# Kernel optimization log

Hardware: AMD Instinct MI355X
Metric: run time of the kernel (lower is better)

## Reference

```python
import jax, jax.numpy as jnp
import numpy as np

B, IN_DIM, C, E, TOPK = 16384, 768, 50, 8, 2
RH = 256          # router hidden_dim
HS = [512, 256]   # expert hidden_sizes
THR = 0.05        # BitNet-1.58b ternarization threshold


def _xavier(k, shape):
    fan_out, fan_in = shape[-2], shape[-1]
    lim = float(np.sqrt(6.0 / (fan_in + fan_out)))
    return jax.random.uniform(k, shape, jnp.float32, -lim, lim)


def setup_inputs() -> dict:
    key = jax.random.key(0)
    ks = jax.random.split(key, 8)
    return {
        "x": jax.random.normal(ks[0], (B, IN_DIM), jnp.float32),
        # Router MLP: in_dim -> RH -> RH//2 -> E (torch Linear: W is (out,in))
        "rW1": _xavier(ks[1], (RH, IN_DIM)), "rb1": jnp.zeros((RH,), jnp.float32),
        "rW2": _xavier(ks[2], (RH // 2, RH)), "rb2": jnp.zeros((RH // 2,), jnp.float32),
        "rW3": _xavier(ks[3], (E, RH // 2)), "rb3": jnp.zeros((E,), jnp.float32),
        # Stacked expert weights: (E, out, in)
        "eW1": _xavier(ks[4], (E, HS[0], IN_DIM)), "eb1": jnp.zeros((E, HS[0]), jnp.float32),
        "eW2": _xavier(ks[5], (E, HS[1], HS[0])), "eb2": jnp.zeros((E, HS[1]), jnp.float32),
        "eW3": _xavier(ks[6], (E, C, HS[1])), "eb3": jnp.zeros((E, C), jnp.float32),
    }


def _ternary(W):
    # BitNet-1.58b: ternarize weights with |w|>threshold, scale by mean |W| per matrix
    scale = jnp.mean(jnp.abs(W), axis=(-2, -1), keepdims=True)
    Wq = jnp.sign(W) * (jnp.abs(W) > THR).astype(W.dtype)
    return Wq * scale


def reference(x, rW1, rb1, rW2, rb2, rW3, rb3, eW1, eb1, eW2, eb2, eW3, eb3):
    # ---- Router (eval mode: dropout = identity) ----
    h = jax.nn.relu(x @ rW1.T + rb1)
    h = jax.nn.relu(h @ rW2.T + rb2)
    router_logits = h @ rW3.T + rb3                      # (B, E)
    router_p = jax.nn.softmax(router_logits, axis=1)     # (B, E)

    # ---- Top-k gating; scatter gate weights back to dense (B, E) ----
    k_val, k_idx = jax.lax.top_k(router_p, TOPK)         # (B, K)
    rows = jnp.arange(x.shape[0])[:, None]
    gate = jnp.zeros_like(router_p).at[rows, k_idx].set(k_val)  # 0 for unselected experts

    # ---- Batched ternary-quantized expert MLPs (all experts, all samples) ----
    W1q, W2q, W3q = _ternary(eW1), _ternary(eW2), _ternary(eW3)
    a1 = jax.nn.relu(jnp.einsum('bd,ehd->ebh', x, W1q) + eb1[:, None, :])   # (E,B,H1)
    a2 = jax.nn.relu(jnp.einsum('ebh,egh->ebg', a1, W2q) + eb2[:, None, :]) # (E,B,H2)
    expert_logits = jnp.einsum('ebg,ecg->ebc', a2, W3q) + eb3[:, None, :]   # (E,B,C)

    # ---- Weighted combine over top-k experts (equivalent to the per-expert loop) ----
    out = jnp.einsum('ebc,be->bc', expert_logits, gate) / TOPK              # (B,C)

    lb_loss = jnp.float32(0.0)  # eval mode: self.training is False
    return (out, router_p, lb_loss)
```

## Files before the change

kernel.cpp:

```cpp
#include <hip/hip_runtime.h>
#include <hip/hip_bf16.h>

typedef __attribute__((ext_vector_type(4))) float f32x4;
typedef __attribute__((ext_vector_type(8))) short bf16x8;

#define B_ROWS 16384
#define IN_DIM 768
#define H1 512
#define H2 256
#define NC 50
#define NE 8
#define RH1 256
#define RH2 128
#define CHK 128

static __device__ __forceinline__ f32x4 mfma16(bf16x8 a, bf16x8 b, f32x4 c) {
    return __builtin_amdgcn_mfma_f32_16x16x32_bf16(a, b, c, 0, 0, 0);
}

typedef __attribute__((address_space(1))) const unsigned int gas_u32;
typedef __attribute__((address_space(3))) unsigned int las_u32;
static __device__ __forceinline__ void gl16(const void* g, void* l) {
    __builtin_amdgcn_global_load_lds((gas_u32*)g, (las_u32*)l, 16, 0, 0);
}

static __device__ __forceinline__ bf16x8 expand_frag(uint2 pw) {
    unsigned q0 = (pw.x & 0x01010101u) << 7;
    unsigned q1 = (pw.y & 0x01010101u) << 7;
    union { unsigned u[4]; bf16x8 v; } r;
    r.u[0] = __builtin_amdgcn_perm(pw.x, q0, 0x05010400u);
    r.u[1] = __builtin_amdgcn_perm(pw.x, q0, 0x07030602u);
    r.u[2] = __builtin_amdgcn_perm(pw.y, q1, 0x05010400u);
    r.u[3] = __builtin_amdgcn_perm(pw.y, q1, 0x07030602u);
    return r.v;
}

static __device__ __forceinline__ void decomp_f4(float4 v, ushort4* hv, ushort4* lv) {
    float vv[4] = {v.x, v.y, v.z, v.w};
    ushort ho[4], lo4[4];
    #pragma unroll
    for (int q = 0; q < 4; ++q) {
        __hip_bfloat16 h = __float2bfloat16(vv[q]);
        float hf = __bfloat162float(h);
        __hip_bfloat16 l = __float2bfloat16(vv[q] - hf);
        ho[q] = *(ushort*)&h; lo4[q] = *(ushort*)&l;
    }
    *hv = make_ushort4(ho[0], ho[1], ho[2], ho[3]);
    *lv = make_ushort4(lo4[0], lo4[1], lo4[2], lo4[3]);
}

static __device__ __forceinline__ ushort4 cvt_f4_bf16(float4 v) {
    float vv[4] = {v.x, v.y, v.z, v.w};
    ushort ho[4];
    #pragma unroll
    for (int q = 0; q < 4; ++q) {
        __hip_bfloat16 h = __float2bfloat16(vv[q]);
        ho[q] = *(ushort*)&h;
    }
    return make_ushort4(ho[0], ho[1], ho[2], ho[3]);
}

__global__ __launch_bounds__(512) void pack_absum_kernel(
    const float* __restrict__ eW1, const float* __restrict__ eW2, const float* __restrict__ eW3,
    unsigned char* __restrict__ W1p8, unsigned char* __restrict__ W2p8,
    unsigned char* __restrict__ W3p8,
    float* __restrict__ p1, float* __restrict__ p2, float* __restrict__ p3)
{
    const int mat = blockIdx.y >> 3, e = blockIdx.y & 7;
    const int u = blockIdx.x * 512 + threadIdx.x;
    const float* src; unsigned char* dst; int valid = 1; float* P; int np;
    if (mat == 0) {
        int lane = u & 63, nblk = (u >> 6) & 31, ks = u >> 11;
        int n = nblk * 16 + (lane & 15), k = ks * 32 + (lane >> 4) * 8;
        src = eW1 + ((size_t)e * H1 + n) * IN_DIM + k;
        dst = W1p8 + (size_t)e * 393216
            + (size_t)ks * 16384 + (nblk >> 1) * 1024 + lane * 16 + (nblk & 1) * 8;
        P = p1; np = 96;
    } else if (mat == 1) {
        if (u >= 16384) return;
        int lane = u & 63, nblk = (u >> 6) & 15, ks = u >> 10;
        int n = nblk * 16 + (lane & 15), k = ks * 32 + (lane >> 4) * 8;
        src = eW2 + ((size_t)e * H2 + n) * H1 + k;
        dst = W2p8 + (size_t)e * 131072
            + (size_t)ks * 8192 + (nblk >> 1) * 1024 + lane * 16 + (nblk & 1) * 8;
        P = p2; np = 32;
    } else {
        if (u >= 2048) return;
        int lane = u & 63, nblk = (u >> 6) & 3, ks = u >> 8;
        int n = nblk * 16 + (lane & 15), k = ks * 32 + (lane >> 4) * 8;
        valid = (n < NC);
        src = eW3 + ((size_t)e * NC + (valid ? n : 0)) * H2 + k;
        dst = W3p8 + ((size_t)e * 2048 + u) * 8;
        P = p3; np = 4;
    }
    unsigned lo = 0, hi = 0;
    float s = 0.f;
    #pragma unroll
    for (int j = 0; j < 4; ++j) {
        float w = valid ? src[j] : 0.f;
        s += fabsf(w);
        unsigned c = (fabsf(w) > 0.05f) ? (w > 0.f ? 0x3Fu : 0xBFu) : 0u;
        lo |= c << (8 * j);
    }
    #pragma unroll
    for (int j = 0; j < 4; ++j) {
        float w = valid ? src[4 + j] : 0.f;
        s += fabsf(w);
        unsigned c = (fabsf(w) > 0.05f) ? (w > 0.f ? 0x3Fu : 0xBFu) : 0u;
        hi |= c << (8 * j);
    }
    *(uint2*)dst = make_uint2(lo, hi);
    const int lane = threadIdx.x & 63, wave = threadIdx.x >> 6;
    #pragma unroll
    for (int o = 32; o; o >>= 1) s += __shfl_down(s, o);
    __shared__ float red[8];
    if (lane == 0) red[wave] = s;
    __syncthreads();
    if (threadIdx.x == 0) {
        float t = 0.f;
        #pragma unroll
        for (int i = 0; i < 8; ++i) t += red[i];
        P[e * np + blockIdx.x] = t;
    }
}

__global__ __launch_bounds__(64) void finalize_scales_kernel(
    const float* __restrict__ p1, const float* __restrict__ p2, const float* __restrict__ p3,
    float* __restrict__ s1, float* __restrict__ s2, float* __restrict__ s3,
    int* __restrict__ counts)
{
    int t = threadIdx.x;
    if (t < 8) {
        float a = 0.f;
        for (int i = 0; i < 96; ++i) a += p1[t * 96 + i];
        s1[t] = a / (float)(H1 * IN_DIM);
    } else if (t < 16) {
        int e = t - 8; float a = 0.f;
        for (int i = 0; i < 32; ++i) a += p2[e * 32 + i];
        s2[e] = a / (float)(H2 * H1);
    } else if (t < 24) {
        int e = t - 16; float a = 0.f;
        for (int i = 0; i < 4; ++i) a += p3[e * 4 + i];
        s3[e] = a / (float)(NC * H2);
    } else if (t < 32) {
        counts[t - 24] = 0;
    }
}

__global__ __launch_bounds__(512) void pack_router_kernel(
    const float* __restrict__ rW1, ushort* __restrict__ rw1hp, ushort* __restrict__ rw1lp,
    const float* __restrict__ rW2, ushort* __restrict__ rw2hp, ushort* __restrict__ rw2lp)
{
    int u = blockIdx.x * 512 + threadIdx.x;
    const float* src; ushort* dh; ushort* dl;
    if (u < 24576) {
        int lane = u & 63, nblk = (u >> 6) & 15, ks = u >> 10;
        int n = nblk * 16 + (lane & 15), k = ks * 32 + (lane >> 4) * 8;
        src = rW1 + (size_t)n * IN_DIM + k;
        dh = rw1hp + (size_t)u * 8; dl = rw1lp + (size_t)u * 8;
    } else {
        int v = u - 24576;
        if (v >= 4096) return;
        int lane = v & 63, nblk = (v >> 6) & 7, ks = v >> 9;
        int n = nblk * 16 + (lane & 15), k = ks * 32 + (lane >> 4) * 8;
        src = rW2 + (size_t)n * RH1 + k;
        dh = rw2hp + (size_t)v * 8; dl = rw2lp + (size_t)v * 8;
    }
    ushort oh[8], ol[8];
    #pragma unroll
    for (int j = 0; j < 8; ++j) {
        float w = src[j];
        __hip_bfloat16 h = __float2bfloat16(w);
        float hf = __bfloat162float(h);
        __hip_bfloat16 l = __float2bfloat16(w - hf);
        oh[j] = *(ushort*)&h; ol[j] = *(ushort*)&l;
    }
    ((ushort4*)dh)[0] = make_ushort4(oh[0], oh[1], oh[2], oh[3]);
    ((ushort4*)dh)[1] = make_ushort4(oh[4], oh[5], oh[6], oh[7]);
    ((ushort4*)dl)[0] = make_ushort4(ol[0], ol[1], ol[2], ol[3]);
    ((ushort4*)dl)[1] = make_ushort4(ol[4], ol[5], ol[6], ol[7]);
}

__global__ __launch_bounds__(1024) void router_fused_kernel(
    const float* __restrict__ x,
    const ushort* __restrict__ rw1hp, const ushort* __restrict__ rw1lp, const float* __restrict__ rb1,
    const ushort* __restrict__ rw2hp, const ushort* __restrict__ rw2lp, const float* __restrict__ rb2,
    const float* __restrict__ rW3, const float* __restrict__ rb3,
    float* __restrict__ router_p, float* __restrict__ gate,
    float* __restrict__ lb_out, int* __restrict__ t2)
{
    __shared__ __align__(16) unsigned char smem[134144];
    unsigned char* Wst = smem;
    ushort (*Xdh)[32][136] = (ushort(*)[32][136])(smem + 65536);
    ushort (*Xdl)[32][136] = (ushort(*)[32][136])(smem + 65536 + 17408);
    float (*h2s)[132]      = (float(*)[132])(smem + 65536);
    ushort (*h1hs)[264]    = (ushort(*)[264])(smem + 100352);
    ushort (*h1ls)[264]    = (ushort(*)[264])(smem + 117248);

    const int tid = threadIdx.x, wave = tid >> 6, lane = tid & 63;
    const int lm = lane & 15, lk = lane >> 4;
    const int r0 = blockIdx.x * 32;

    const int srow = tid >> 5;
    const int sc4r = (tid & 31) * 4;
    const float* sg = x + (size_t)(r0 + srow) * IN_DIM + sc4r;

    float4 sv = *(const float4*)sg;
    gl16(rw1hp + tid * 8, Wst + tid * 16);
    gl16(rw1lp + tid * 8, Wst + 16384 + tid * 16);
    {
        ushort4 hv, lv;
        decomp_f4(sv, &hv, &lv);
        *(ushort4*)&Xdh[0][srow][sc4r] = hv;
        *(ushort4*)&Xdl[0][srow][sc4r] = lv;
    }
    __syncthreads();

    {
        f32x4 acc[2] = {};
        for (int s = 0; s < 24; ++s) {
            const int c = s >> 2;
            const unsigned char* curh = Wst + (s & 1) * 32768;
            const unsigned char* curl = curh + 16384;
            if (s + 1 < 24) {
                unsigned char* dst = Wst + ((s + 1) & 1) * 32768;
                gl16(rw1hp + (size_t)(s + 1) * 8192 + tid * 8, dst + tid * 16);
                gl16(rw1lp + (size_t)(s + 1) * 8192 + tid * 8, dst + 16384 + tid * 16);
            } else {
                if (tid < 512) gl16(rw2hp + tid * 8, Wst + tid * 16);
                else           gl16(rw2lp + (tid & 511) * 8, Wst + 16384 + (tid & 511) * 16);
            }
            if ((s & 3) == 0 && c < 5)
                sv = *(const float4*)(sg + (c + 1) * CHK);
            const ushort (*Xch)[136] = Xdh[c & 1];
            const ushort (*Xcl)[136] = Xdl[c & 1];
            const int ko = (s & 3) * 32 + lk * 8;
            bf16x8 ah0 = *(const bf16x8*)&Xch[lm][ko];
            bf16x8 al0 = *(const bf16x8*)&Xcl[lm][ko];
            bf16x8 ah1 = *(const bf16x8*)&Xch[16 + lm][ko];
            bf16x8 al1 = *(const bf16x8*)&Xcl[16 + lm][ko];
            bf16x8 bh = *(const bf16x8*)(curh + (wave * 64 + lane) * 16);
            bf16x8 bl = *(const bf16x8*)(curl + (wave * 64 + lane) * 16);
            acc[0] = mfma16(ah0, bh, acc[0]);
            acc[0] = mfma16(ah0, bl, acc[0]);
            acc[0] = mfma16(al0, bh, acc[0]);
            acc[1] = mfma16(ah1, bh, acc[1]);
            acc[1] = mfma16(ah1, bl, acc[1]);
            acc[1] = mfma16(al1, bh, acc[1]);
            if ((s & 3) == 2 && c < 5) {
                ushort4 hv, lv;
                decomp_f4(sv, &hv, &lv);
                *(ushort4*)&Xdh[(c + 1) & 1][srow][sc4r] = hv;
                *(ushort4*)&Xdl[(c + 1) & 1][srow][sc4r] = lv;
            }
            __syncthreads();
        }
        int col = wave * 16 + lm;
        float bv = rb1[col];
        #pragma unroll
        for (int m = 0; m < 2; ++m)
            #pragma unroll
            for (int r = 0; r < 4; ++r) {
                float v = acc[m][r] + bv;
                v = v > 0.f ? v : 0.f;
                __hip_bfloat16 h = __float2bfloat16(v);
                float hf = __bfloat162float(h);
                __hip_bfloat16 l = __float2bfloat16(v - hf);
                int row = m * 16 + lk * 4 + r;
                h1hs[row][col] = *(ushort*)&h;
                h1ls[row][col] = *(ushort*)&l;
            }
    }
    __syncthreads();

    {
        const int mt = wave >> 3, nb = wave & 7;
        f32x4 acc2 = {};
        for (int s = 0; s < 8; ++s) {
            const unsigned char* curh = Wst + (s & 1) * 32768;
            const unsigned char* curl = curh + 16384;
            if (s + 1 < 8) {
                unsigned char* dst = Wst + ((s + 1) & 1) * 32768;
                if (tid < 512) gl16(rw2hp + (size_t)(s + 1) * 4096 + tid * 8, dst + tid * 16);
                else           gl16(rw2lp + (size_t)(s + 1) * 4096 + (tid & 511) * 8, dst + 16384 + (tid & 511) * 16);
            }
            const int ko = s * 32 + lk * 8;
            bf16x8 ah = *(const bf16x8*)&h1hs[mt * 16 + lm][ko];
            bf16x8 al = *(const bf16x8*)&h1ls[mt * 16 + lm][ko];
            bf16x8 bh = *(const bf16x8*)(curh + (nb * 64 + lane) * 16);
            bf16x8 bl = *(const bf16x8*)(curl + (nb * 64 + lane) * 16);
            acc2 = mfma16(ah, bh, acc2);
            acc2 = mfma16(ah, bl, acc2);
            acc2 = mfma16(al, bh, acc2);
            __syncthreads();
        }
        int col2 = nb * 16 + lm;
        float bv = rb2[col2];
        #pragma unroll
        for (int r = 0; r < 4; ++r) {
            float v = acc2[r] + bv;
            h2s[mt * 16 + lk * 4 + r][col2] = v > 0.f ? v : 0.f;
        }
    }
    __syncthreads();

    const int o = lane >> 3, kq = lane & 7;
    #pragma unroll
    for (int i = 0; i < 2; ++i) {
        int rloc = wave * 2 + i;
        int b = r0 + rloc;
        float s = 0.f;
        #pragma unroll
        for (int q = 0; q < 4; ++q) {
            float4 hv = *(const float4*)&h2s[rloc][kq * 16 + q * 4];
            float4 wv = *(const float4*)&rW3[o * RH2 + kq * 16 + q * 4];
            s += hv.x * wv.x + hv.y * wv.y + hv.z * wv.z + hv.w * wv.w;
        }
        s += __shfl_xor(s, 1);
        s += __shfl_xor(s, 2);
        s += __shfl_xor(s, 4);
        float logit = s + rb3[o];
        float l[8];
        #pragma unroll
        for (int j = 0; j < 8; ++j) l[j] = __shfl(logit, j * 8);
        float m = l[0];
        #pragma unroll
        for (int j = 1; j < 8; ++j) m = fmaxf(m, l[j]);
        float p[8]; float sum = 0.f;
        #pragma unroll
        for (int j = 0; j < 8; ++j) { p[j] = expf(l[j] - m); sum += p[j]; }
        float inv = 1.f / sum;
        #pragma unroll
        for (int j = 0; j < 8; ++j) p[j] *= inv;
        int i1 = 0; float v1 = p[0];
        #pragma unroll
        for (int j = 1; j < 8; ++j) if (p[j] > v1) { v1 = p[j]; i1 = j; }
        int i2 = -1; float v2 = -1.f;
        #pragma unroll
        for (int j = 0; j < 8; ++j) if (j != i1 && p[j] > v2) { v2 = p[j]; i2 = j; }
        if (lane < 8) {
            router_p[(size_t)b * 8 + lane] = p[lane];
            float gv = (lane == i1) ? v1 * 0.5f : ((lane == i2) ? v2 * 0.5f : 0.f);
            gate[(size_t)b * 8 + lane] = gv;
        }
        if (lane == 0) t2[b] = i1 | (i2 << 8);
    }
    if (blockIdx.x == 0 && tid == 0) lb_out[0] = 0.f;
}

__global__ __launch_bounds__(256) void build_lists_kernel(
    const int* __restrict__ t2, int* __restrict__ counts, int* __restrict__ ent)
{
    __shared__ int hist[8], base[8];
    const int r = blockIdx.x * 256 + threadIdx.x;
    if (threadIdx.x < 8) hist[threadIdx.x] = 0;
    __syncthreads();
    const int v = t2[r];
    const int i1 = v & 255, i2 = v >> 8;
    const int rk1 = atomicAdd(&hist[i1], 1);
    const int rk2 = atomicAdd(&hist[i2], 1);
    __syncthreads();
    if (threadIdx.x < 8) base[threadIdx.x] = atomicAdd(&counts[threadIdx.x], hist[threadIdx.x]);
    __syncthreads();
    ent[i1 * B_ROWS + base[i1] + rk1] = (r << 1);
    ent[i2 * B_ROWS + base[i2] + rk2] = (r << 1) | 1;
}

__global__ __launch_bounds__(1024) void expert_fused_kernel(
    const float* __restrict__ x,
    const unsigned char* __restrict__ W1p8, const unsigned char* __restrict__ W2p8,
    const unsigned char* __restrict__ W3p8,
    const float* __restrict__ s1, const float* __restrict__ s2, const float* __restrict__ s3,
    const float* __restrict__ eb1, const float* __restrict__ eb2, const float* __restrict__ eb3,
    const float* __restrict__ gate,
    const int* __restrict__ counts, const int* __restrict__ ent,
    float* __restrict__ S0, float* __restrict__ S1)
{
    int pfx[9]; pfx[0] = 0;
    #pragma unroll
    for (int i = 0; i < 8; ++i) pfx[i + 1] = pfx[i] + ((counts[i] + 63) >> 6);
    const int T = pfx[8];
    const int R = (T + 7) >> 3;
    const int xcd = blockIdx.x & 7, j = blockIdx.x >> 3;
    if (j >= R) return;
    const int g = xcd * R + j;
    if (g >= T) return;
    int e = 0;
    #pragma unroll
    for (int i = 0; i < 7; ++i) if (g >= pfx[i + 1]) e = i + 1;
    const int t = g - pfx[e];
    const int cnt = counts[e];

    __shared__ __align__(16) unsigned char smem[101376];
    __hip_bfloat16 (*A1s)[520] = (__hip_bfloat16(*)[520])(smem);
    __hip_bfloat16 (*A2s)[264] = (__hip_bfloat16(*)[264])(smem + 66560);
    ushort (*Xd)[64][136]      = (ushort(*)[64][136])(smem + 66560);
    __shared__ int rowL[64];
    __shared__ int slotL[64];
    __shared__ float gL[64];

    const int tid = threadIdx.x;
    const int wave = tid >> 6;
    const int lane = tid & 63;
    const int lm = lane & 15;
    const int lk = lane >> 4;

    if (tid < 64) {
        int idx = t * 64 + tid;
        if (idx < cnt) {
            int entv = ent[e * B_ROWS + idx];
            int r = entv >> 1;
            rowL[tid] = r;
            slotL[tid] = entv & 1;
            gL[tid] = gate[(size_t)r * NE + e];
        } else {
            rowL[tid] = -1; slotL[tid] = 0; gL[tid] = 0.f;
        }
    }
    __syncthreads();

    const int srow = tid >> 4;
    const int sc8  = (tid & 15) * 8;
    int SR = rowL[srow]; if (SR < 0) SR = 0;
    const float* sg = x + (size_t)SR * IN_DIM + sc8;
    const unsigned char* Wsrc1 = W1p8 + (size_t)e * 393216;
    const unsigned char* Wsrc2 = W2p8 + (size_t)e * 131072;
    const unsigned char* Wsrc3 = W3p8 + (size_t)e * 16384;

    {
        float4 fa = *(const float4*)(sg);
        float4 fb = *(const float4*)(sg + 4);
        *(ushort4*)&Xd[0][srow][sc8]     = cvt_f4_bf16(fa);
        *(ushort4*)&Xd[0][srow][sc8 + 4] = cvt_f4_bf16(fb);
    }
    __syncthreads();

    {
        f32x4 acc[4][2] = {};
        const int w2 = wave * 2;
        const unsigned char* wp1 = Wsrc1 + wave * 1024 + lane * 16;
        uint4 pw[4];
        #pragma unroll
        for (int k = 0; k < 4; ++k)
            pw[k] = *(const uint4*)(wp1 + (size_t)k * 16384);
        for (int i = 0; i < 6; ++i) {
            float4 fa, fb;
            if (i + 1 < 6) {
                fa = *(const float4*)(sg + (i + 1) * CHK);
                fb = *(const float4*)(sg + (i + 1) * CHK + 4);
            }
            uint4 cur[4];
            #pragma unroll
            for (int k = 0; k < 4; ++k) cur[k] = pw[k];
            if (i + 1 < 6) {
                #pragma unroll
                for (int k = 0; k < 4; ++k)
                    pw[k] = *(const uint4*)(wp1 + (size_t)(4 * i + 4 + k) * 16384);
            }
            const ushort (*Xc)[136] = Xd[i & 1];
            #pragma unroll
            for (int k4 = 0; k4 < 4; ++k4) {
                const int ko = k4 * 32 + lk * 8;
                bf16x8 a0 = *(const bf16x8*)&Xc[     lm][ko];
                bf16x8 a1 = *(const bf16x8*)&Xc[16 + lm][ko];
                bf16x8 a2 = *(const bf16x8*)&Xc[32 + lm][ko];
                bf16x8 a3 = *(const bf16x8*)&Xc[48 + lm][ko];
                bf16x8 b0 = expand_frag(make_uint2(cur[k4].x, cur[k4].y));
                bf16x8 b1 = expand_frag(make_uint2(cur[k4].z, cur[k4].w));
                acc[0][0] = mfma16(a0, b0, acc[0][0]);
                acc[1][0] = mfma16(a1, b0, acc[1][0]);
                acc[2][0] = mfma16(a2, b0, acc[2][0]);
                acc[3][0] = mfma16(a3, b0, acc[3][0]);
                acc[0][1] = mfma16(a0, b1, acc[0][1]);
                acc[1][1] = mfma16(a1, b1, acc[1][1]);
                acc[2][1] = mfma16(a2, b1, acc[2][1]);
                acc[3][1] = mfma16(a3, b1, acc[3][1]);
            }
            if (i + 1 < 6) {
                *(ushort4*)&Xd[(i + 1) & 1][srow][sc8]     = cvt_f4_bf16(fa);
                *(ushort4*)&Xd[(i + 1) & 1][srow][sc8 + 4] = cvt_f4_bf16(fb);
            }
            __syncthreads();
        }
        const float* bias = eb1 + e * H1;
        const float sc = s1[e];
        #pragma unroll
        for (int n = 0; n < 2; ++n) {
            int ncol = (w2 + n) * 16 + lm;
            float bv = bias[ncol];
            #pragma unroll
            for (int m = 0; m < 4; ++m)
                #pragma unroll
                for (int r = 0; r < 4; ++r) {
                    float v = fmaf(acc[m][n][r], sc, bv);
                    v = v > 0.f ? v : 0.f;
                    A1s[m * 16 + lk * 4 + r][ncol] = __float2bfloat16(v);
                }
        }
    }
    __syncthreads();

    {
        const int mt = wave >> 3, ntw = wave & 7;
        const unsigned char* wp2 = Wsrc2 + ntw * 1024 + lane * 16;
        f32x4 acc[2][2] = {};
        uint4 pwa = *(const uint4*)(wp2);
        uint4 pwb = *(const uint4*)(wp2 + 8192);
        for (int s = 0; s < 16; s += 2) {
            uint4 c0 = pwa, c1 = pwb;
            if (s + 2 < 16) {
                pwa = *(const uint4*)(wp2 + (size_t)(s + 2) * 8192);
                pwb = *(const uint4*)(wp2 + (size_t)(s + 3) * 8192);
            }
            {
                const int ko = s * 32 + lk * 8;
                bf16x8 a0 = *(const bf16x8*)&A1s[mt * 32 +      lm][ko];
                bf16x8 a1 = *(const bf16x8*)&A1s[mt * 32 + 16 + lm][ko];
                bf16x8 b0 = expand_frag(make_uint2(c0.x, c0.y));
                bf16x8 b1 = expand_frag(make_uint2(c0.z, c0.w));
                acc[0][0] = mfma16(a0, b0, acc[0][0]);
                acc[1][0] = mfma16(a1, b0, acc[1][0]);
                acc[0][1] = mfma16(a0, b1, acc[0][1]);
                acc[1][1] = mfma16(a1, b1, acc[1][1]);
            }
            {
                const int ko = (s + 1) * 32 + lk * 8;
                bf16x8 a0 = *(const bf16x8*)&A1s[mt * 32 +      lm][ko];
                bf16x8 a1 = *(const bf16x8*)&A1s[mt * 32 + 16 + lm][ko];
                bf16x8 b0 = expand_frag(make_uint2(c1.x, c1.y));
                bf16x8 b1 = expand_frag(make_uint2(c1.z, c1.w));
                acc[0][0] = mfma16(a0, b0, acc[0][0]);
                acc[1][0] = mfma16(a1, b0, acc[1][0]);
                acc[0][1] = mfma16(a0, b1, acc[0][1]);
                acc[1][1] = mfma16(a1, b1, acc[1][1]);
            }
        }
        const float* bias = eb2 + e * H2;
        const float sc = s2[e];
        #pragma unroll
        for (int n = 0; n < 2; ++n) {
            int ncol = (ntw * 2 + n) * 16 + lm;
            float bv = bias[ncol];
            #pragma unroll
            for (int m = 0; m < 2; ++m)
                #pragma unroll
                for (int r = 0; r < 4; ++r) {
                    float v = fmaf(acc[m][n][r], sc, bv);
                    v = v > 0.f ? v : 0.f;
                    A2s[mt * 32 + m * 16 + lk * 4 + r][ncol] = __float2bfloat16(v);
                }
        }
    }
    __syncthreads();

    {
        const int mt = wave & 3, nt = wave >> 2;
        f32x4 acc = {};
        #pragma unroll
        for (int s = 0; s < 8; ++s) {
            bf16x8 a = *(const bf16x8*)&A2s[mt * 16 + lm][s * 32 + lk * 8];
            uint2 pw = *(const uint2*)(Wsrc3 + ((s * 4 + nt) * 64 + lane) * 8);
            bf16x8 b = expand_frag(pw);
            acc = mfma16(a, b, acc);
        }
        int col = nt * 16 + lm;
        if (col < NC) {
            const float bv = eb3[e * NC + col];
            const float sc = s3[e];
            #pragma unroll
            for (int r = 0; r < 4; ++r) {
                int row = mt * 16 + lk * 4 + r;
                int R2 = rowL[row];
                if (R2 >= 0) {
                    float v = gL[row] * fmaf(acc[r], sc, bv);
                    float* Sb = slotL[row] ? S1 : S0;
                    Sb[(size_t)R2 * 64 + col] = v;
                }
            }
        }
    }
}

__global__ __launch_bounds__(256) void combine_kernel(
    const float* __restrict__ S0, const float* __restrict__ S1, float* __restrict__ out)
{
    int i = blockIdx.x * 256 + threadIdx.x;
    if (i < B_ROWS * NC) {
        int row = i / NC, col = i % NC;
        out[i] = S0[(size_t)row * 64 + col] + S1[(size_t)row * 64 + col];
    }
}

extern "C" void kernel_launch(void* const* d_in, const int* in_sizes, int n_in,
                              void* d_out, int out_size, void* d_ws, size_t ws_size,
                              hipStream_t stream) {
    const float* x   = (const float*)d_in[0];
    const float* rW1 = (const float*)d_in[1];
    const float* rb1 = (const float*)d_in[2];
    const float* rW2 = (const float*)d_in[3];
    const float* rb2 = (const float*)d_in[4];
    const float* rW3 = (const float*)d_in[5];
    const float* rb3 = (const float*)d_in[6];
    const float* eW1 = (const float*)d_in[7];
    const float* eb1 = (const float*)d_in[8];
    const float* eW2 = (const float*)d_in[9];
    const float* eb2 = (const float*)d_in[10];
    const float* eW3 = (const float*)d_in[11];
    const float* eb3 = (const float*)d_in[12];

    float* out_main = (float*)d_out;
    float* router_p = out_main + (size_t)B_ROWS * NC;
    float* lb_out   = router_p + (size_t)B_ROWS * NE;

    char* ws = (char*)d_ws;
    size_t off = 0;
    unsigned char* W1p8 = (unsigned char*)(ws + off); off += (size_t)NE * 49152 * 8;
    unsigned char* W2p8 = (unsigned char*)(ws + off); off += (size_t)NE * 16384 * 8;
    unsigned char* W3p8 = (unsigned char*)(ws + off); off += (size_t)NE * 2048 * 8;
    float* S0   = (float*)(ws + off);  off += (size_t)B_ROWS * 64 * 4;
    float* S1   = (float*)(ws + off);  off += (size_t)B_ROWS * 64 * 4;
    ushort* rw1hp = (ushort*)(ws + off); off += (size_t)24576 * 8 * 2;
    ushort* rw1lp = (ushort*)(ws + off); off += (size_t)24576 * 8 * 2;
    ushort* rw2hp = (ushort*)(ws + off); off += (size_t)4096 * 8 * 2;
    ushort* rw2lp = (ushort*)(ws + off); off += (size_t)4096 * 8 * 2;
    float* gate = (float*)(ws + off);  off += (size_t)B_ROWS * NE * 4;
    int*   ent  = (int*)(ws + off);    off += (size_t)NE * B_ROWS * 4;
    int*   t2   = (int*)(ws + off);    off += (size_t)B_ROWS * 4;
    int* counts = (int*)(ws + off);    off += 256;
    float* s1   = (float*)(ws + off);  off += 256;
    float* s2   = (float*)(ws + off);  off += 256;
    float* s3   = (float*)(ws + off);  off += 256;
    float* p1   = (float*)(ws + off);  off += NE * 96 * 4;
    float* p2   = (float*)(ws + off);  off += NE * 32 * 4;
    float* p3   = (float*)(ws + off);  off += NE * 4 * 4;

    pack_absum_kernel<<<dim3(96, 24), 512, 0, stream>>>(
        eW1, eW2, eW3, W1p8, W2p8, W3p8, p1, p2, p3);
    pack_router_kernel<<<56, 512, 0, stream>>>(rW1, rw1hp, rw1lp, rW2, rw2hp, rw2lp);
    finalize_scales_kernel<<<1, 64, 0, stream>>>(p1, p2, p3, s1, s2, s3, counts);

    router_fused_kernel<<<B_ROWS / 32, 1024, 0, stream>>>(
        x, rw1hp, rw1lp, rb1, rw2hp, rw2lp, rb2, rW3, rb3, router_p, gate, lb_out, t2);
    build_lists_kernel<<<B_ROWS / 256, 256, 0, stream>>>(t2, counts, ent);

    expert_fused_kernel<<<1024, 1024, 0, stream>>>(
        x, W1p8, W2p8, W3p8, s1, s2, s3, eb1, eb2, eb3, gate, counts, ent, S0, S1);
    combine_kernel<<<(B_ROWS * NC + 255) / 256, 256, 0, stream>>>(S0, S1, out_main);
}
```

Measured before the change: 140.6 us.

## Load router weights directly into registers instead of staging through LDS

The router MLP's first two layers now fetch pre-packed bf16 hi/lo weight fragments straight from global memory into registers, prefetched one chunk ahead. This replaces the double-buffered global_load_lds staging and removes most per-step __syncthreads. Shared memory drops from about 134KB to about 68KB, which could allow more resident blocks. In exchange, register pressure rises and the router blocks read weights redundantly through L2 rather than sharing them in LDS.

```diff
diff --git a/kernel.cpp b/kernel.cpp
--- a/kernel.cpp
+++ b/kernel.cpp
@@ -16,12 +16,6 @@
 
 static __device__ __forceinline__ f32x4 mfma16(bf16x8 a, bf16x8 b, f32x4 c) {
     return __builtin_amdgcn_mfma_f32_16x16x32_bf16(a, b, c, 0, 0, 0);
-}
-
-typedef __attribute__((address_space(1))) const unsigned int gas_u32;
-typedef __attribute__((address_space(3))) unsigned int las_u32;
-static __device__ __forceinline__ void gl16(const void* g, void* l) {
-    __builtin_amdgcn_global_load_lds((gas_u32*)g, (las_u32*)l, 16, 0, 0);
 }
 
 static __device__ __forceinline__ bf16x8 expand_frag(uint2 pw) {
@@ -189,13 +183,12 @@
     float* __restrict__ router_p, float* __restrict__ gate,
     float* __restrict__ lb_out, int* __restrict__ t2)
 {
-    __shared__ __align__(16) unsigned char smem[134144];
-    unsigned char* Wst = smem;
-    ushort (*Xdh)[32][136] = (ushort(*)[32][136])(smem + 65536);
-    ushort (*Xdl)[32][136] = (ushort(*)[32][136])(smem + 65536 + 17408);
-    float (*h2s)[132]      = (float(*)[132])(smem + 65536);
-    ushort (*h1hs)[264]    = (ushort(*)[264])(smem + 100352);
-    ushort (*h1ls)[264]    = (ushort(*)[264])(smem + 117248);
+    __shared__ __align__(16) unsigned char smem[68608];
+    ushort (*Xdh)[32][136] = (ushort(*)[32][136])(smem);
+    ushort (*Xdl)[32][136] = (ushort(*)[32][136])(smem + 17408);
+    ushort (*h1hs)[264]    = (ushort(*)[264])(smem + 34816);
+    ushort (*h1ls)[264]    = (ushort(*)[264])(smem + 51712);
+    float (*h2s)[132]      = (float(*)[132])(smem);
 
     const int tid = threadIdx.x, wave = tid >> 6, lane = tid & 63;
     const int lm = lane & 15, lk = lane >> 4;
@@ -205,10 +198,8 @@
     const int sc4r = (tid & 31) * 4;
     const float* sg = x + (size_t)(r0 + srow) * IN_DIM + sc4r;
 
-    float4 sv = *(const float4*)sg;
-    gl16(rw1hp + tid * 8, Wst + tid * 16);
-    gl16(rw1lp + tid * 8, Wst + 16384 + tid * 16);
     {
+        float4 sv = *(const float4*)sg;
         ushort4 hv, lv;
         decomp_f4(sv, &hv, &lv);
         *(ushort4*)&Xdh[0][srow][sc4r] = hv;
@@ -218,40 +209,45 @@
 
     {
         f32x4 acc[2] = {};
-        for (int s = 0; s < 24; ++s) {
-            const int c = s >> 2;
-            const unsigned char* curh = Wst + (s & 1) * 32768;
-            const unsigned char* curl = curh + 16384;
-            if (s + 1 < 24) {
-                unsigned char* dst = Wst + ((s + 1) & 1) * 32768;
-                gl16(rw1hp + (size_t)(s + 1) * 8192 + tid * 8, dst + tid * 16);
-                gl16(rw1lp + (size_t)(s + 1) * 8192 + tid * 8, dst + 16384 + tid * 16);
-            } else {
-                if (tid < 512) gl16(rw2hp + tid * 8, Wst + tid * 16);
-                else           gl16(rw2lp + (tid & 511) * 8, Wst + 16384 + (tid & 511) * 16);
-            }
-            if ((s & 3) == 0 && c < 5)
-                sv = *(const float4*)(sg + (c + 1) * CHK);
-            const ushort (*Xch)[136] = Xdh[c & 1];
-            const ushort (*Xcl)[136] = Xdl[c & 1];
-            const int ko = (s & 3) * 32 + lk * 8;
-            bf16x8 ah0 = *(const bf16x8*)&Xch[lm][ko];
-            bf16x8 al0 = *(const bf16x8*)&Xcl[lm][ko];
-            bf16x8 ah1 = *(const bf16x8*)&Xch[16 + lm][ko];
-            bf16x8 al1 = *(const bf16x8*)&Xcl[16 + lm][ko];
-            bf16x8 bh = *(const bf16x8*)(curh + (wave * 64 + lane) * 16);
-            bf16x8 bl = *(const bf16x8*)(curl + (wave * 64 + lane) * 16);
-            acc[0] = mfma16(ah0, bh, acc[0]);
-            acc[0] = mfma16(ah0, bl, acc[0]);
-            acc[0] = mfma16(al0, bh, acc[0]);
-            acc[1] = mfma16(ah1, bh, acc[1]);
-            acc[1] = mfma16(ah1, bl, acc[1]);
-            acc[1] = mfma16(al1, bh, acc[1]);
-            if ((s & 3) == 2 && c < 5) {
+        const ushort* wph = rw1hp + (size_t)(wave * 64 + lane) * 8;
+        const ushort* wpl = rw1lp + (size_t)(wave * 64 + lane) * 8;
+        uint4 ph[4], pl[4];
+        #pragma unroll
+        for (int k = 0; k < 4; ++k) {
+            ph[k] = *(const uint4*)(wph + (size_t)k * 8192);
+            pl[k] = *(const uint4*)(wpl + (size_t)k * 8192);
+        }
+        for (int i = 0; i < 6; ++i) {
+            float4 sv;
+            if (i + 1 < 6) sv = *(const float4*)(sg + (i + 1) * CHK);
+            const ushort (*Xch)[136] = Xdh[i & 1];
+            const ushort (*Xcl)[136] = Xdl[i & 1];
+            #pragma unroll
+            for (int k4 = 0; k4 < 4; ++k4) {
+                uint4 ch = ph[k4], cl = pl[k4];
+                if (i + 1 < 6) {
+                    ph[k4] = *(const uint4*)(wph + (size_t)(4 * i + 4 + k4) * 8192);
+                    pl[k4] = *(const uint4*)(wpl + (size_t)(4 * i + 4 + k4) * 8192);
+                }
+                const int ko = k4 * 32 + lk * 8;
+                bf16x8 ah0 = *(const bf16x8*)&Xch[lm][ko];
+                bf16x8 al0 = *(const bf16x8*)&Xcl[lm][ko];
+                bf16x8 ah1 = *(const bf16x8*)&Xch[16 + lm][ko];
+                bf16x8 al1 = *(const bf16x8*)&Xcl[16 + lm][ko];
+                bf16x8 bh = *(bf16x8*)&ch;
+                bf16x8 bl = *(bf16x8*)&cl;
+                acc[0] = mfma16(ah0, bh, acc[0]);
+                acc[0] = mfma16(ah0, bl, acc[0]);
+                acc[0] = mfma16(al0, bh, acc[0]);
+                acc[1] = mfma16(ah1, bh, acc[1]);
+                acc[1] = mfma16(ah1, bl, acc[1]);
+                acc[1] = mfma16(al1, bh, acc[1]);
+            }
+            if (i + 1 < 6) {
                 ushort4 hv, lv;
                 decomp_f4(sv, &hv, &lv);
-                *(ushort4*)&Xdh[(c + 1) & 1][srow][sc4r] = hv;
-                *(ushort4*)&Xdl[(c + 1) & 1][srow][sc4r] = lv;
+                *(ushort4*)&Xdh[(i + 1) & 1][srow][sc4r] = hv;
+                *(ushort4*)&Xdl[(i + 1) & 1][srow][sc4r] = lv;
             }
             __syncthreads();
         }
@@ -275,25 +271,43 @@
 
     {
         const int mt = wave >> 3, nb = wave & 7;
+        const ushort* w2h = rw2hp + (size_t)(nb * 64 + lane) * 8;
+        const ushort* w2l = rw2lp + (size_t)(nb * 64 + lane) * 8;
         f32x4 acc2 = {};
-        for (int s = 0; s < 8; ++s) {
-            const unsigned char* curh = Wst + (s & 1) * 32768;
-            const unsigned char* curl = curh + 16384;
-            if (s + 1 < 8) {
-                unsigned char* dst = Wst + ((s + 1) & 1) * 32768;
-                if (tid < 512) gl16(rw2hp + (size_t)(s + 1) * 4096 + tid * 8, dst + tid * 16);
-                else           gl16(rw2lp + (size_t)(s + 1) * 4096 + (tid & 511) * 8, dst + 16384 + (tid & 511) * 16);
-            }
-            const int ko = s * 32 + lk * 8;
-            bf16x8 ah = *(const bf16x8*)&h1hs[mt * 16 + lm][ko];
-            bf16x8 al = *(const bf16x8*)&h1ls[mt * 16 + lm][ko];
-            bf16x8 bh = *(const bf16x8*)(curh + (nb * 64 + lane) * 16);
-            bf16x8 bl = *(const bf16x8*)(curl + (nb * 64 + lane) * 16);
-            acc2 = mfma16(ah, bh, acc2);
-            acc2 = mfma16(ah, bl, acc2);
-            acc2 = mfma16(al, bh, acc2);
-            __syncthreads();
-        }
+        uint4 pha = *(const uint4*)(w2h);
+        uint4 pla = *(const uint4*)(w2l);
+        uint4 phb = *(const uint4*)(w2h + 4096);
+        uint4 plb = *(const uint4*)(w2l + 4096);
+        for (int s = 0; s < 8; s += 2) {
+            uint4 cha = pha, cla = pla, chb = phb, clb = plb;
+            if (s + 2 < 8) {
+                pha = *(const uint4*)(w2h + (size_t)(s + 2) * 4096);
+                pla = *(const uint4*)(w2l + (size_t)(s + 2) * 4096);
+                phb = *(const uint4*)(w2h + (size_t)(s + 3) * 4096);
+                plb = *(const uint4*)(w2l + (size_t)(s + 3) * 4096);
+            }
+            {
+                const int ko = s * 32 + lk * 8;
+                bf16x8 ah = *(const bf16x8*)&h1hs[mt * 16 + lm][ko];
+                bf16x8 al = *(const bf16x8*)&h1ls[mt * 16 + lm][ko];
+                bf16x8 bh = *(bf16x8*)&cha;
+                bf16x8 bl = *(bf16x8*)&cla;
+                acc2 = mfma16(ah, bh, acc2);
+                acc2 = mfma16(ah, bl, acc2);
+                acc2 = mfma16(al, bh, acc2);
+            }
+            {
+                const int ko = (s + 1) * 32 + lk * 8;
+                bf16x8 ah = *(const bf16x8*)&h1hs[mt * 16 + lm][ko];
+                bf16x8 al = *(const bf16x8*)&h1ls[mt * 16 + lm][ko];
+                bf16x8 bh = *(bf16x8*)&chb;
+                bf16x8 bl = *(bf16x8*)&clb;
+                acc2 = mfma16(ah, bh, acc2);
+                acc2 = mfma16(ah, bl, acc2);
+                acc2 = mfma16(al, bh, acc2);
+            }
+        }
+        __syncthreads();
         int col2 = nb * 16 + lm;
         float bv = rb2[col2];
         #pragma unroll
```

After: 124.8 us. 1.13x faster.
